# Performance work log

Measured on AMD Instinct MI355X. Metric: run time of the kernel, lower is better.

## Reference

```python
import jax, jax.numpy as jnp
import numpy as np

B, N, E = 4, 4096, 65536
FIN, FOUT = 128, 64
ALPHA = 0.2          # LeakyReLU negative slope
NEG = -9e15          # mask value from original code


def setup_inputs() -> dict:
    key = jax.random.key(0)
    k1, k2, k3, k4 = jax.random.split(key, 4)
    h = jax.random.normal(k1, (B, N, FIN), dtype=jnp.float32)
    edge_index = jax.random.randint(k2, (B, 2, E), 0, N, dtype=jnp.int32)
    # Xavier-uniform-like params
    W = jax.random.uniform(k3, (FIN, FOUT), jnp.float32, -1.0, 1.0) * (1.414 * np.sqrt(6.0 / (FIN + FOUT)))
    a = jax.random.uniform(k4, (2 * FOUT, 1), jnp.float32, -1.0, 1.0) * (1.414 * np.sqrt(6.0 / (2 * FOUT + 1)))
    return {"h": h, "edge_index": edge_index, "W": W, "a": a}


def reference(h, edge_index, W, a):
    # Wh: [B, N, FOUT]
    Wh = jnp.einsum('bnf,fo->bno', h, W)
    Wh_flat = Wh.reshape(-1, FOUT)  # [B*N, FOUT]

    # Faithful to original: raw node ids (< N) index the flattened tensor,
    # i.e. edge features are gathered from batch 0's rows.
    src = edge_index[:, 0].reshape(-1)  # [B*E]
    tgt = edge_index[:, 1].reshape(-1)  # [B*E]
    a_input = jnp.concatenate([Wh_flat[src], Wh_flat[tgt]], axis=1)  # [B*E, 2*FOUT]
    e = (a_input @ a)[:, 0]  # [B*E]

    b_idx = jnp.repeat(jnp.arange(B), E)
    e_dense = jnp.zeros((B, N, N), e.dtype).at[b_idx, src, tgt].set(e)
    e_dense = jax.nn.leaky_relu(e_dense, ALPHA)

    attention = jnp.where(e_dense > 0, e_dense, NEG)
    attention = jax.nn.softmax(attention, axis=1)  # softmax over dim=1 as in original
    # dropout p=0.0 -> no-op

    h_prime = jnp.einsum('bmn,bnf->bmf', attention, Wh)  # [B, N, FOUT]
    return jax.nn.elu(h_prime)  # concat=True path
```

## Files before the change

kernel.cpp:

```cpp
#include <hip/hip_runtime.h>
#include <hip/hip_bf16.h>

#define BB 4
#define NN 4096
#define EE 65536
#define FIN 128
#define FOUT 64
#define CAP 64

__device__ __forceinline__ unsigned enc_f32(float f) {
    unsigned b = __float_as_uint(f);
    return (b & 0x80000000u) ? ~b : (b | 0x80000000u);
}
__device__ __forceinline__ float dec_f32(unsigned e) {
    unsigned b = (e & 0x80000000u) ? (e & 0x7FFFFFFFu) : ~e;
    return __uint_as_float(b);
}

__global__ __launch_bounds__(256) void phase0_kernel(
        const float* __restrict__ h, const float* __restrict__ W, const float* __restrict__ a,
        float* __restrict__ Wh, int* __restrict__ deg, unsigned* __restrict__ Menc,
        float* __restrict__ D, float* __restrict__ base,
        float* __restrict__ as_, float* __restrict__ at_) {
    __shared__ union {
        struct { float hs[32][132]; float Ws[64][64]; } wh;
        float Wa[256];
    } smem;
    int tid = threadIdx.x;
    int bid = blockIdx.x;
    if (bid < 512) {
        long row0 = (long)bid * 32;
        for (int i = tid; i < 1024; i += 256) {
            float4 v = ((const float4*)(h + row0 * FIN))[i];
            int r = (i * 4) >> 7, c = (i * 4) & 127;
            *(float4*)&smem.wh.hs[r][c] = v;
        }
        int tx = tid & 15, ty = tid >> 4;
        int c0 = tx * 4, r0 = ty * 2;
        float acc[2][4] = {};
        for (int kk = 0; kk < 128; kk += 64) {
            __syncthreads();
            for (int i = tid; i < 1024; i += 256) {
                float4 v = ((const float4*)(W + kk * FOUT))[i];
                int k = (i * 4) >> 6, c = (i * 4) & 63;
                *(float4*)&smem.wh.Ws[k][c] = v;
            }
            __syncthreads();
#pragma unroll
            for (int k = 0; k < 64; k += 4) {
                float4 w0 = *(const float4*)&smem.wh.Ws[k][c0];
                float4 w1 = *(const float4*)&smem.wh.Ws[k + 1][c0];
                float4 w2 = *(const float4*)&smem.wh.Ws[k + 2][c0];
                float4 w3 = *(const float4*)&smem.wh.Ws[k + 3][c0];
#pragma unroll
                for (int r = 0; r < 2; ++r) {
                    float4 hv = *(const float4*)&smem.wh.hs[r0 + r][kk + k];
                    acc[r][0] += hv.x * w0.x + hv.y * w1.x + hv.z * w2.x + hv.w * w3.x;
                    acc[r][1] += hv.x * w0.y + hv.y * w1.y + hv.z * w2.y + hv.w * w3.y;
                    acc[r][2] += hv.x * w0.z + hv.y * w1.z + hv.z * w2.z + hv.w * w3.z;
                    acc[r][3] += hv.x * w0.w + hv.y * w1.w + hv.z * w2.w + hv.w * w3.w;
                }
            }
        }
#pragma unroll
        for (int r = 0; r < 2; ++r)
            *(float4*)&Wh[(row0 + r0 + r) * FOUT + c0] = *(float4*)&acc[r][0];
    } else {
        int local = bid - 512;
        int gid2 = local * 256 + tid;
        if (gid2 < BB * NN) { deg[gid2] = 0; Menc[gid2] = 0u; D[gid2] = 0.f; }
        if (gid2 < BB * FOUT) base[gid2] = 0.f;
        {
            int half = tid >> 7, k = tid & 127;
            const float* wr = W + k * FOUT;
            const float* av = a + half * FOUT;
            float s = 0.f;
#pragma unroll
            for (int f2 = 0; f2 < FOUT; ++f2) s += wr[f2] * av[f2];
            smem.Wa[half * 128 + k] = s;
        }
        __syncthreads();
        int lane = tid & 63, wv = tid >> 6;
#pragma unroll
        for (int r = 0; r < 2; ++r) {
            int n = local * 8 + wv * 2 + r;
            float h0v = h[(long)n * FIN + lane];
            float h1v = h[(long)n * FIN + 64 + lane];
            float ps = h0v * smem.Wa[lane] + h1v * smem.Wa[64 + lane];
            float pt = h0v * smem.Wa[128 + lane] + h1v * smem.Wa[192 + lane];
            for (int off = 32; off; off >>= 1) {
                ps += __shfl_down(ps, off);
                pt += __shfl_down(pt, off);
            }
            if (lane == 0) { as_[n] = ps; at_[n] = pt; }
        }
    }
}

__global__ void edge_kernel(const int* __restrict__ ei, const float* __restrict__ as_,
                            const float* __restrict__ at_, unsigned* __restrict__ Menc,
                            int* __restrict__ deg, int* __restrict__ csr) {
    int idx = blockIdx.x * 256 + threadIdx.x;
    int b = idx >> 16;
    int j = idx & 65535;
    const int* eb = ei + (long)b * 2 * EE;
    int s = eb[j], t = eb[EE + j];
    float as_s = as_[s];
    if (as_s + at_[t] > 0.f) {
        int row = (b << 12) | s;
        atomicMax(&Menc[(b << 12) | t], enc_f32(as_s));
        int slot = atomicAdd(&deg[row], 1);
        if (slot < CAP) csr[row * CAP + slot] = t;
    }
}

__global__ void phase2_kernel(int* __restrict__ deg, int* __restrict__ csr,
                              const float* __restrict__ as_, const unsigned* __restrict__ Menc,
                              float* __restrict__ D, const float* __restrict__ Wh,
                              float* __restrict__ base) {
    __shared__ float red[4][64];
    int tid = threadIdx.x;
    int lane = tid & 63;
    int row = blockIdx.x * 4 + (tid >> 6);
    int b = row >> 12, s = row & 4095;
    int draw = min(deg[row], CAP);
    int t = -1;
    if (lane < draw) t = csr[row * CAP + lane];
    bool dup = false;
    for (int k = 0; k < draw; ++k) {
        int tk = __shfl(t, k);
        if (k < lane && tk == t) dup = true;
    }
    bool keep = (lane < draw) && !dup;
    unsigned long long mask = __ballot(keep);
    int pfx = __popcll(mask & ((1ull << lane) - 1ull));
    if (keep) {
        csr[row * CAP + pfx] = t;
        float M = dec_f32(Menc[(b << 12) | t]);
        atomicAdd(&D[(b << 12) | t], expf(as_[s] - M));
    }
    if (lane == 0) deg[row] = __popcll(mask);

    if (blockIdx.x < 128) {
        int bb = blockIdx.x >> 5, chunk = blockIdx.x & 31;
        int f = tid & 63, ty = tid >> 6;
        float acc = 0.f;
        int t0 = chunk * (NN / 32);
        for (int tt = t0 + ty; tt < t0 + NN / 32; tt += 4)
            if (Menc[(bb << 12) | tt] == 0u) acc += Wh[(((long)bb << 12) | tt) * FOUT + f];
        red[ty][f] = acc;
        __syncthreads();
        if (ty == 0)
            atomicAdd(&base[(bb << 6) | f],
                      (red[0][f] + red[1][f] + red[2][f] + red[3][f]) * (1.0f / NN));
    }
}

__global__ void gather_kernel(const int* __restrict__ deg, const int* __restrict__ csr,
                              const float* __restrict__ as_, const unsigned* __restrict__ Menc,
                              const float* __restrict__ D, const float* __restrict__ Wh,
                              const float* __restrict__ base, float* __restrict__ out) {
    int tid = threadIdx.x;
    int lane = tid & 63;
    int row = blockIdx.x * 4 + (tid >> 6);
    int b = row >> 12, s = row & 4095;
    int d = deg[row];
    float as_s = as_[s];
    float acc = 0.f;
    const int* cr = csr + row * CAP;
    const float* Whb = Wh + (((long)b << 12) * FOUT);
    for (int j = 0; j < d; ++j) {
        int t = cr[j];
        float M = dec_f32(Menc[(b << 12) | t]);
        float w = expf(as_s - M) / D[(b << 12) | t];
        acc += w * Whb[t * FOUT + lane];
    }
    float x = acc + base[(b << 6) | lane];
    out[(long)row * FOUT + lane] = x > 0.f ? x : expm1f(x);
}

extern "C" void kernel_launch(void* const* d_in, const int* in_sizes, int n_in,
                              void* d_out, int out_size, void* d_ws, size_t ws_size,
                              hipStream_t stream) {
    const float* h  = (const float*)d_in[0];
    const int*   ei = (const int*)d_in[1];
    const float* W  = (const float*)d_in[2];
    const float* a  = (const float*)d_in[3];
    float* out = (float*)d_out;

    char* ws = (char*)d_ws;
    float*    Wh   = (float*)(ws);
    int*      csr  = (int*)(ws + 4194304);
    int*      deg  = (int*)(ws + 8388608);
    unsigned* Menc = (unsigned*)(ws + 8454144);
    float*    D    = (float*)(ws + 8519680);
    float*    as_  = (float*)(ws + 8585216);
    float*    at_  = (float*)(ws + 8601600);
    float*    base = (float*)(ws + 8617984);

    phase0_kernel<<<1024, 256, 0, stream>>>(h, W, a, Wh, deg, Menc, D, base, as_, at_);
    edge_kernel<<<(BB * EE) / 256, 256, 0, stream>>>(ei, as_, at_, Menc, deg, csr);
    phase2_kernel<<<(BB * NN) / 4, 256, 0, stream>>>(deg, csr, as_, Menc, D, Wh, base);
    gather_kernel<<<(BB * NN) / 4, 256, 0, stream>>>(deg, csr, as_, Menc, D, Wh, base, out);
}
```

Before: 88.20 us.

## Fuse four kernels into one persistent kernel with grid barriers

Merges the projection, edge scoring, dedup/normalisation and gather kernels into a single persistent kernel of 256 blocks that separates phases with atomic grid-wide barriers, plus a tiny init kernel. It also drops the per-target max stabiliser (atomicMax on an encoded float) in favour of a plain flag and unshifted exp(as_s), and processes four rows at once in the gather loop for more memory-level parallelism. The aim is to cut launch overhead and atomic traffic. The trade-offs are spin-barrier cost, lower parallelism from a fixed 256-block grid, possible overflow of exp without the max shift, and a deadlock risk if not all blocks are co-resident.

Result: slower. 345.2 us (+291.4%).

```diff
diff --git a/kernel.cpp b/kernel.cpp
--- a/kernel.cpp
+++ b/kernel.cpp
@@ -7,69 +7,84 @@
 #define FIN 128
 #define FOUT 64
 #define CAP 64
-
-__device__ __forceinline__ unsigned enc_f32(float f) {
-    unsigned b = __float_as_uint(f);
-    return (b & 0x80000000u) ? ~b : (b | 0x80000000u);
-}
-__device__ __forceinline__ float dec_f32(unsigned e) {
-    unsigned b = (e & 0x80000000u) ? (e & 0x7FFFFFFFu) : ~e;
-    return __uint_as_float(b);
-}
-
-__global__ __launch_bounds__(256) void phase0_kernel(
-        const float* __restrict__ h, const float* __restrict__ W, const float* __restrict__ a,
-        float* __restrict__ Wh, int* __restrict__ deg, unsigned* __restrict__ Menc,
-        float* __restrict__ D, float* __restrict__ base,
-        float* __restrict__ as_, float* __restrict__ at_) {
+#define GRID 256
+
+__device__ __forceinline__ void gbar(unsigned* c) {
+    __syncthreads();
+    if (threadIdx.x == 0) {
+        __hip_atomic_fetch_add(c, 1u, __ATOMIC_ACQ_REL, __HIP_MEMORY_SCOPE_AGENT);
+        while (__hip_atomic_fetch_add(c, 0u, __ATOMIC_ACQUIRE,
+                                      __HIP_MEMORY_SCOPE_AGENT) < (unsigned)GRID)
+            __builtin_amdgcn_s_sleep(8);
+    }
+    __syncthreads();
+}
+
+__global__ void init_kernel(unsigned* __restrict__ bar, float* __restrict__ base) {
+    if (threadIdx.x < 3) bar[threadIdx.x] = 0u;
+    base[threadIdx.x] = 0.f;
+}
+
+__global__ __launch_bounds__(256, 2) void fused(
+        const float* __restrict__ h, const int* __restrict__ ei,
+        const float* __restrict__ W, const float* __restrict__ a,
+        float* __restrict__ out, float* __restrict__ Wh, int* __restrict__ csr,
+        int* __restrict__ deg, unsigned* __restrict__ flag, float* __restrict__ D,
+        float* __restrict__ as_, float* __restrict__ at_, float* __restrict__ base,
+        unsigned* __restrict__ bar) {
     __shared__ union {
         struct { float hs[32][132]; float Ws[64][64]; } wh;
         float Wa[256];
+        float red[4][64];
     } smem;
     int tid = threadIdx.x;
     int bid = blockIdx.x;
-    if (bid < 512) {
-        long row0 = (long)bid * 32;
-        for (int i = tid; i < 1024; i += 256) {
-            float4 v = ((const float4*)(h + row0 * FIN))[i];
-            int r = (i * 4) >> 7, c = (i * 4) & 127;
-            *(float4*)&smem.wh.hs[r][c] = v;
-        }
+    int lane = tid & 63, wv = tid >> 6;
+
+    {
+        int gz = bid * 256 + tid;
+        if (gz < BB * NN) { deg[gz] = 0; flag[gz] = 0u; D[gz] = 0.f; }
+
         int tx = tid & 15, ty = tid >> 4;
         int c0 = tx * 4, r0 = ty * 2;
-        float acc[2][4] = {};
-        for (int kk = 0; kk < 128; kk += 64) {
+        for (int tile = bid; tile < 512; tile += GRID) {
             __syncthreads();
+            long row0 = (long)tile * 32;
             for (int i = tid; i < 1024; i += 256) {
-                float4 v = ((const float4*)(W + kk * FOUT))[i];
-                int k = (i * 4) >> 6, c = (i * 4) & 63;
-                *(float4*)&smem.wh.Ws[k][c] = v;
-            }
-            __syncthreads();
-#pragma unroll
-            for (int k = 0; k < 64; k += 4) {
-                float4 w0 = *(const float4*)&smem.wh.Ws[k][c0];
-                float4 w1 = *(const float4*)&smem.wh.Ws[k + 1][c0];
-                float4 w2 = *(const float4*)&smem.wh.Ws[k + 2][c0];
-                float4 w3 = *(const float4*)&smem.wh.Ws[k + 3][c0];
-#pragma unroll
-                for (int r = 0; r < 2; ++r) {
-                    float4 hv = *(const float4*)&smem.wh.hs[r0 + r][kk + k];
-                    acc[r][0] += hv.x * w0.x + hv.y * w1.x + hv.z * w2.x + hv.w * w3.x;
-                    acc[r][1] += hv.x * w0.y + hv.y * w1.y + hv.z * w2.y + hv.w * w3.y;
-                    acc[r][2] += hv.x * w0.z + hv.y * w1.z + hv.z * w2.z + hv.w * w3.z;
-                    acc[r][3] += hv.x * w0.w + hv.y * w1.w + hv.z * w2.w + hv.w * w3.w;
+                float4 v = ((const float4*)(h + row0 * FIN))[i];
+                int r = (i * 4) >> 7, c = (i * 4) & 127;
+                *(float4*)&smem.wh.hs[r][c] = v;
+            }
+            float acc[2][4] = {};
+            for (int kk = 0; kk < 128; kk += 64) {
+                __syncthreads();
+                for (int i = tid; i < 1024; i += 256) {
+                    float4 v = ((const float4*)(W + kk * FOUT))[i];
+                    int k = (i * 4) >> 6, c = (i * 4) & 63;
+                    *(float4*)&smem.wh.Ws[k][c] = v;
                 }
-            }
-        }
-#pragma unroll
-        for (int r = 0; r < 2; ++r)
-            *(float4*)&Wh[(row0 + r0 + r) * FOUT + c0] = *(float4*)&acc[r][0];
-    } else {
-        int local = bid - 512;
-        int gid2 = local * 256 + tid;
-        if (gid2 < BB * NN) { deg[gid2] = 0; Menc[gid2] = 0u; D[gid2] = 0.f; }
-        if (gid2 < BB * FOUT) base[gid2] = 0.f;
+                __syncthreads();
+#pragma unroll
+                for (int k = 0; k < 64; k += 4) {
+                    float4 w0 = *(const float4*)&smem.wh.Ws[k][c0];
+                    float4 w1 = *(const float4*)&smem.wh.Ws[k + 1][c0];
+                    float4 w2 = *(const float4*)&smem.wh.Ws[k + 2][c0];
+                    float4 w3 = *(const float4*)&smem.wh.Ws[k + 3][c0];
+#pragma unroll
+                    for (int r = 0; r < 2; ++r) {
+                        float4 hv = *(const float4*)&smem.wh.hs[r0 + r][kk + k];
+                        acc[r][0] += hv.x * w0.x + hv.y * w1.x + hv.z * w2.x + hv.w * w3.x;
+                        acc[r][1] += hv.x * w0.y + hv.y * w1.y + hv.z * w2.y + hv.w * w3.y;
+                        acc[r][2] += hv.x * w0.z + hv.y * w1.z + hv.z * w2.z + hv.w * w3.z;
+                        acc[r][3] += hv.x * w0.w + hv.y * w1.w + hv.z * w2.w + hv.w * w3.w;
+                    }
+                }
+            }
+#pragma unroll
+            for (int r = 0; r < 2; ++r)
+                *(float4*)&Wh[(row0 + r0 + r) * FOUT + c0] = *(float4*)&acc[r][0];
+        }
+        __syncthreads();
         {
             int half = tid >> 7, k = tid & 127;
             const float* wr = W + k * FOUT;
@@ -80,10 +95,9 @@
             smem.Wa[half * 128 + k] = s;
         }
         __syncthreads();
-        int lane = tid & 63, wv = tid >> 6;
-#pragma unroll
-        for (int r = 0; r < 2; ++r) {
-            int n = local * 8 + wv * 2 + r;
+#pragma unroll
+        for (int r = 0; r < 4; ++r) {
+            int n = bid * 16 + wv * 4 + r;
             float h0v = h[(long)n * FIN + lane];
             float h1v = h[(long)n * FIN + 64 + lane];
             float ps = h0v * smem.Wa[lane] + h1v * smem.Wa[64 + lane];
@@ -95,88 +109,89 @@
             if (lane == 0) { as_[n] = ps; at_[n] = pt; }
         }
     }
-}
-
-__global__ void edge_kernel(const int* __restrict__ ei, const float* __restrict__ as_,
-                            const float* __restrict__ at_, unsigned* __restrict__ Menc,
-                            int* __restrict__ deg, int* __restrict__ csr) {
-    int idx = blockIdx.x * 256 + threadIdx.x;
-    int b = idx >> 16;
-    int j = idx & 65535;
-    const int* eb = ei + (long)b * 2 * EE;
-    int s = eb[j], t = eb[EE + j];
-    float as_s = as_[s];
-    if (as_s + at_[t] > 0.f) {
-        int row = (b << 12) | s;
-        atomicMax(&Menc[(b << 12) | t], enc_f32(as_s));
-        int slot = atomicAdd(&deg[row], 1);
-        if (slot < CAP) csr[row * CAP + slot] = t;
-    }
-}
-
-__global__ void phase2_kernel(int* __restrict__ deg, int* __restrict__ csr,
-                              const float* __restrict__ as_, const unsigned* __restrict__ Menc,
-                              float* __restrict__ D, const float* __restrict__ Wh,
-                              float* __restrict__ base) {
-    __shared__ float red[4][64];
-    int tid = threadIdx.x;
-    int lane = tid & 63;
-    int row = blockIdx.x * 4 + (tid >> 6);
-    int b = row >> 12, s = row & 4095;
-    int draw = min(deg[row], CAP);
-    int t = -1;
-    if (lane < draw) t = csr[row * CAP + lane];
-    bool dup = false;
-    for (int k = 0; k < draw; ++k) {
-        int tk = __shfl(t, k);
-        if (k < lane && tk == t) dup = true;
-    }
-    bool keep = (lane < draw) && !dup;
-    unsigned long long mask = __ballot(keep);
-    int pfx = __popcll(mask & ((1ull << lane) - 1ull));
-    if (keep) {
-        csr[row * CAP + pfx] = t;
-        float M = dec_f32(Menc[(b << 12) | t]);
-        atomicAdd(&D[(b << 12) | t], expf(as_[s] - M));
-    }
-    if (lane == 0) deg[row] = __popcll(mask);
-
-    if (blockIdx.x < 128) {
-        int bb = blockIdx.x >> 5, chunk = blockIdx.x & 31;
+    gbar(&bar[0]);
+
+#pragma unroll
+    for (int b = 0; b < BB; ++b) {
+        int j = bid * 256 + tid;
+        const int* eb = ei + (long)b * 2 * EE;
+        int s = eb[j], t = eb[EE + j];
+        float as_s = as_[s];
+        if (as_s + at_[t] > 0.f) {
+            flag[(b << 12) | t] = 1u;
+            int row = (b << 12) | s;
+            int slot = atomicAdd(&deg[row], 1);
+            if (slot < CAP) csr[row * CAP + slot] = t;
+        }
+    }
+    gbar(&bar[1]);
+
+    for (int i = 0; i < 16; ++i) {
+        int row = bid * 64 + wv * 16 + i;
+        int b = row >> 12, s = row & 4095;
+        int draw = min(deg[row], CAP);
+        int t = -1;
+        if (lane < draw) t = csr[row * CAP + lane];
+        bool dup = false;
+        for (int k = 0; k < draw; ++k) {
+            int tk = __shfl(t, k);
+            if (k < lane && tk == t) dup = true;
+        }
+        bool keep = (lane < draw) && !dup;
+        unsigned long long mask = __ballot(keep);
+        int pfx = __popcll(mask & ((1ull << lane) - 1ull));
+        if (keep) {
+            csr[row * CAP + pfx] = t;
+            atomicAdd(&D[(b << 12) | t], expf(as_[s]));
+        }
+        if (lane == 0) deg[row] = __popcll(mask);
+    }
+    if (bid < 128) {
+        int bb = bid >> 5, chunk = bid & 31;
         int f = tid & 63, ty = tid >> 6;
         float acc = 0.f;
         int t0 = chunk * (NN / 32);
         for (int tt = t0 + ty; tt < t0 + NN / 32; tt += 4)
-            if (Menc[(bb << 12) | tt] == 0u) acc += Wh[(((long)bb << 12) | tt) * FOUT + f];
-        red[ty][f] = acc;
+            if (flag[(bb << 12) | tt] == 0u) acc += Wh[(((long)bb << 12) | tt) * FOUT + f];
+        __syncthreads();
+        smem.red[ty][f] = acc;
         __syncthreads();
         if (ty == 0)
             atomicAdd(&base[(bb << 6) | f],
-                      (red[0][f] + red[1][f] + red[2][f] + red[3][f]) * (1.0f / NN));
-    }
-}
-
-__global__ void gather_kernel(const int* __restrict__ deg, const int* __restrict__ csr,
-                              const float* __restrict__ as_, const unsigned* __restrict__ Menc,
-                              const float* __restrict__ D, const float* __restrict__ Wh,
-                              const float* __restrict__ base, float* __restrict__ out) {
-    int tid = threadIdx.x;
-    int lane = tid & 63;
-    int row = blockIdx.x * 4 + (tid >> 6);
-    int b = row >> 12, s = row & 4095;
-    int d = deg[row];
-    float as_s = as_[s];
-    float acc = 0.f;
-    const int* cr = csr + row * CAP;
-    const float* Whb = Wh + (((long)b << 12) * FOUT);
-    for (int j = 0; j < d; ++j) {
-        int t = cr[j];
-        float M = dec_f32(Menc[(b << 12) | t]);
-        float w = expf(as_s - M) / D[(b << 12) | t];
-        acc += w * Whb[t * FOUT + lane];
-    }
-    float x = acc + base[(b << 6) | lane];
-    out[(long)row * FOUT + lane] = x > 0.f ? x : expm1f(x);
+                      (smem.red[0][f] + smem.red[1][f] + smem.red[2][f] + smem.red[3][f]) *
+                          (1.0f / NN));
+    }
+    gbar(&bar[2]);
+
+    {
+        int b = bid >> 6;
+        const float* Whb = Wh + (((long)b << 12) * FOUT);
+        const float* Db = D + (b << 12);
+        float bs = base[(b << 6) | lane];
+        for (int rr = 0; rr < 16; rr += 4) {
+            int row0 = bid * 64 + wv * 16 + rr;
+            int d0 = deg[row0], d1 = deg[row0 + 1], d2 = deg[row0 + 2], d3 = deg[row0 + 3];
+            float E0 = expf(as_[row0 & 4095]), E1 = expf(as_[(row0 + 1) & 4095]);
+            float E2 = expf(as_[(row0 + 2) & 4095]), E3 = expf(as_[(row0 + 3) & 4095]);
+            const int* c0p = csr + (long)row0 * CAP;
+            const int* c1p = c0p + CAP;
+            const int* c2p = c1p + CAP;
+            const int* c3p = c2p + CAP;
+            float a0 = 0.f, a1 = 0.f, a2 = 0.f, a3 = 0.f;
+            int dmax = max(max(d0, d1), max(d2, d3));
+            for (int j = 0; j < dmax; ++j) {
+                if (j < d0) { int t = c0p[j]; a0 += (E0 / Db[t]) * Whb[t * FOUT + lane]; }
+                if (j < d1) { int t = c1p[j]; a1 += (E1 / Db[t]) * Whb[t * FOUT + lane]; }
+                if (j < d2) { int t = c2p[j]; a2 += (E2 / Db[t]) * Whb[t * FOUT + lane]; }
+                if (j < d3) { int t = c3p[j]; a3 += (E3 / Db[t]) * Whb[t * FOUT + lane]; }
+            }
+            float x0 = a0 + bs, x1 = a1 + bs, x2 = a2 + bs, x3 = a3 + bs;
+            out[(long)row0 * FOUT + lane] = x0 > 0.f ? x0 : expm1f(x0);
+            out[(long)(row0 + 1) * FOUT + lane] = x1 > 0.f ? x1 : expm1f(x1);
+            out[(long)(row0 + 2) * FOUT + lane] = x2 > 0.f ? x2 : expm1f(x2);
+            out[(long)(row0 + 3) * FOUT + lane] = x3 > 0.f ? x3 : expm1f(x3);
+        }
+    }
 }
 
 extern "C" void kernel_launch(void* const* d_in, const int* in_sizes, int n_in,
@@ -192,14 +207,14 @@
     float*    Wh   = (float*)(ws);
     int*      csr  = (int*)(ws + 4194304);
     int*      deg  = (int*)(ws + 8388608);
-    unsigned* Menc = (unsigned*)(ws + 8454144);
+    unsigned* flag = (unsigned*)(ws + 8454144);
     float*    D    = (float*)(ws + 8519680);
     float*    as_  = (float*)(ws + 8585216);
     float*    at_  = (float*)(ws + 8601600);
     float*    base = (float*)(ws + 8617984);
-
-    phase0_kernel<<<1024, 256, 0, stream>>>(h, W, a, Wh, deg, Menc, D, base, as_, at_);
-    edge_kernel<<<(BB * EE) / 256, 256, 0, stream>>>(ei, as_, at_, Menc, deg, csr);
-    phase2_kernel<<<(BB * NN) / 4, 256, 0, stream>>>(deg, csr, as_, Menc, D, Wh, base);
-    gather_kernel<<<(BB * NN) / 4, 256, 0, stream>>>(deg, csr, as_, Menc, D, Wh, base, out);
-}
+    unsigned* bar  = (unsigned*)(ws + 8619008);
+
+    init_kernel<<<1, 256, 0, stream>>>(bar, base);
+    fused<<<GRID, 256, 0, stream>>>(h, ei, W, a, out, Wh, csr, deg, flag, D,
+                                    as_, at_, base, bar);
+}
```

## Dedupe edges with a bitmap in edge pass and drop max-subtraction phase

Applied to the files above, without the earlier changes.

Edge duplicates are now removed in the edge kernel with an atomicOr on a per-(batch,src,tgt) bitmap, and the softmax denominator is accumulated there directly as exp(as_s) with no max subtraction. This removes the phase2 kernel and the Menc array. The gather kernel now computes the base term for columns with no entries itself and processes four rows per wave. Each block clears 16KB of a 8MB bitmap, and skipping the max subtraction means exp(as_s) could overflow for large scores.

Result: slower. 104.4 us (+18.4%).

```diff
diff --git a/kernel.cpp b/kernel.cpp
--- a/kernel.cpp
+++ b/kernel.cpp
@@ -8,20 +8,10 @@
 #define FOUT 64
 #define CAP 64
 
-__device__ __forceinline__ unsigned enc_f32(float f) {
-    unsigned b = __float_as_uint(f);
-    return (b & 0x80000000u) ? ~b : (b | 0x80000000u);
-}
-__device__ __forceinline__ float dec_f32(unsigned e) {
-    unsigned b = (e & 0x80000000u) ? (e & 0x7FFFFFFFu) : ~e;
-    return __uint_as_float(b);
-}
-
 __global__ __launch_bounds__(256) void phase0_kernel(
         const float* __restrict__ h, const float* __restrict__ W, const float* __restrict__ a,
-        float* __restrict__ Wh, int* __restrict__ deg, unsigned* __restrict__ Menc,
-        float* __restrict__ D, float* __restrict__ base,
-        float* __restrict__ as_, float* __restrict__ at_) {
+        float* __restrict__ Wh, int* __restrict__ deg, float* __restrict__ D,
+        unsigned* __restrict__ bitmap, float* __restrict__ as_, float* __restrict__ at_) {
     __shared__ union {
         struct { float hs[32][132]; float Ws[64][64]; } wh;
         float Wa[256];
@@ -67,9 +57,10 @@
             *(float4*)&Wh[(row0 + r0 + r) * FOUT + c0] = *(float4*)&acc[r][0];
     } else {
         int local = bid - 512;
+        uint4* bm4 = (uint4*)(bitmap + (long)local * 4096);
+        for (int i = tid; i < 1024; i += 256) bm4[i] = make_uint4(0u, 0u, 0u, 0u);
         int gid2 = local * 256 + tid;
-        if (gid2 < BB * NN) { deg[gid2] = 0; Menc[gid2] = 0u; D[gid2] = 0.f; }
-        if (gid2 < BB * FOUT) base[gid2] = 0.f;
+        if (gid2 < BB * NN) { deg[gid2] = 0; D[gid2] = 0.f; }
         {
             int half = tid >> 7, k = tid & 127;
             const float* wr = W + k * FOUT;
@@ -98,8 +89,9 @@
 }
 
 __global__ void edge_kernel(const int* __restrict__ ei, const float* __restrict__ as_,
-                            const float* __restrict__ at_, unsigned* __restrict__ Menc,
-                            int* __restrict__ deg, int* __restrict__ csr) {
+                            const float* __restrict__ at_, unsigned* __restrict__ bitmap,
+                            int* __restrict__ deg, int* __restrict__ csr,
+                            float* __restrict__ D) {
     int idx = blockIdx.x * 256 + threadIdx.x;
     int b = idx >> 16;
     int j = idx & 65535;
@@ -108,75 +100,70 @@
     float as_s = as_[s];
     if (as_s + at_[t] > 0.f) {
         int row = (b << 12) | s;
-        atomicMax(&Menc[(b << 12) | t], enc_f32(as_s));
-        int slot = atomicAdd(&deg[row], 1);
-        if (slot < CAP) csr[row * CAP + slot] = t;
+        long bit = ((long)row << 12) | t;
+        unsigned m = 1u << (bit & 31);
+        unsigned old = atomicOr(&bitmap[bit >> 5], m);
+        if (!(old & m)) {
+            atomicAdd(&D[(b << 12) | t], expf(as_s));
+            int slot = atomicAdd(&deg[row], 1);
+            if (slot < CAP) csr[row * CAP + slot] = t;
+        }
     }
 }
 
-__global__ void phase2_kernel(int* __restrict__ deg, int* __restrict__ csr,
-                              const float* __restrict__ as_, const unsigned* __restrict__ Menc,
-                              float* __restrict__ D, const float* __restrict__ Wh,
-                              float* __restrict__ base) {
-    __shared__ float red[4][64];
+__global__ __launch_bounds__(256) void gather_kernel(
+        const int* __restrict__ deg, const int* __restrict__ csr,
+        const float* __restrict__ as_, const float* __restrict__ D,
+        const float* __restrict__ Wh, float* __restrict__ out) {
+    __shared__ float bs[64];
+    __shared__ int list[256];
+    __shared__ int cnt;
     int tid = threadIdx.x;
-    int lane = tid & 63;
-    int row = blockIdx.x * 4 + (tid >> 6);
-    int b = row >> 12, s = row & 4095;
-    int draw = min(deg[row], CAP);
-    int t = -1;
-    if (lane < draw) t = csr[row * CAP + lane];
-    bool dup = false;
-    for (int k = 0; k < draw; ++k) {
-        int tk = __shfl(t, k);
-        if (k < lane && tk == t) dup = true;
+    int lane = tid & 63, wv = tid >> 6;
+    int bid = blockIdx.x;
+    int b = bid >> 8;
+    const float* Db = D + (b << 12);
+    const float* Whb = Wh + (((long)b << 12) * FOUT);
+    if (tid == 0) cnt = 0;
+    __syncthreads();
+    for (int i = tid; i < NN; i += 256) {
+        if (Db[i] == 0.f) {
+            int p = atomicAdd(&cnt, 1);
+            if (p < 256) list[p] = i;
+        }
     }
-    bool keep = (lane < draw) && !dup;
-    unsigned long long mask = __ballot(keep);
-    int pfx = __popcll(mask & ((1ull << lane) - 1ull));
-    if (keep) {
-        csr[row * CAP + pfx] = t;
-        float M = dec_f32(Menc[(b << 12) | t]);
-        atomicAdd(&D[(b << 12) | t], expf(as_[s] - M));
+    __syncthreads();
+    if (wv == 0) {
+        int c = min(cnt, 256);
+        float s = 0.f;
+        for (int j = 0; j < c; ++j) s += Whb[list[j] * FOUT + lane];
+        bs[lane] = s * (1.0f / NN);
     }
-    if (lane == 0) deg[row] = __popcll(mask);
+    __syncthreads();
+    float bsv = bs[lane];
 
-    if (blockIdx.x < 128) {
-        int bb = blockIdx.x >> 5, chunk = blockIdx.x & 31;
-        int f = tid & 63, ty = tid >> 6;
-        float acc = 0.f;
-        int t0 = chunk * (NN / 32);
-        for (int tt = t0 + ty; tt < t0 + NN / 32; tt += 4)
-            if (Menc[(bb << 12) | tt] == 0u) acc += Wh[(((long)bb << 12) | tt) * FOUT + f];
-        red[ty][f] = acc;
-        __syncthreads();
-        if (ty == 0)
-            atomicAdd(&base[(bb << 6) | f],
-                      (red[0][f] + red[1][f] + red[2][f] + red[3][f]) * (1.0f / NN));
+    int row0 = bid * 16 + wv * 4;
+    int d0 = min(deg[row0], CAP), d1 = min(deg[row0 + 1], CAP);
+    int d2 = min(deg[row0 + 2], CAP), d3 = min(deg[row0 + 3], CAP);
+    float E0 = expf(as_[row0 & 4095]), E1 = expf(as_[(row0 + 1) & 4095]);
+    float E2 = expf(as_[(row0 + 2) & 4095]), E3 = expf(as_[(row0 + 3) & 4095]);
+    const int* c0p = csr + (long)row0 * CAP;
+    const int* c1p = c0p + CAP;
+    const int* c2p = c1p + CAP;
+    const int* c3p = c2p + CAP;
+    float a0 = 0.f, a1 = 0.f, a2 = 0.f, a3 = 0.f;
+    int dmax = max(max(d0, d1), max(d2, d3));
+    for (int j = 0; j < dmax; ++j) {
+        if (j < d0) { int t = c0p[j]; a0 += (E0 / Db[t]) * Whb[t * FOUT + lane]; }
+        if (j < d1) { int t = c1p[j]; a1 += (E1 / Db[t]) * Whb[t * FOUT + lane]; }
+        if (j < d2) { int t = c2p[j]; a2 += (E2 / Db[t]) * Whb[t * FOUT + lane]; }
+        if (j < d3) { int t = c3p[j]; a3 += (E3 / Db[t]) * Whb[t * FOUT + lane]; }
     }
-}
-
-__global__ void gather_kernel(const int* __restrict__ deg, const int* __restrict__ csr,
-                              const float* __restrict__ as_, const unsigned* __restrict__ Menc,
-                              const float* __restrict__ D, const float* __restrict__ Wh,
-                              const float* __restrict__ base, float* __restrict__ out) {
-    int tid = threadIdx.x;
-    int lane = tid & 63;
-    int row = blockIdx.x * 4 + (tid >> 6);
-    int b = row >> 12, s = row & 4095;
-    int d = deg[row];
-    float as_s = as_[s];
-    float acc = 0.f;
-    const int* cr = csr + row * CAP;
-    const float* Whb = Wh + (((long)b << 12) * FOUT);
-    for (int j = 0; j < d; ++j) {
-        int t = cr[j];
-        float M = dec_f32(Menc[(b << 12) | t]);
-        float w = expf(as_s - M) / D[(b << 12) | t];
-        acc += w * Whb[t * FOUT + lane];
-    }
-    float x = acc + base[(b << 6) | lane];
-    out[(long)row * FOUT + lane] = x > 0.f ? x : expm1f(x);
+    float x0 = a0 + bsv, x1 = a1 + bsv, x2 = a2 + bsv, x3 = a3 + bsv;
+    out[(long)row0 * FOUT + lane] = x0 > 0.f ? x0 : expm1f(x0);
+    out[(long)(row0 + 1) * FOUT + lane] = x1 > 0.f ? x1 : expm1f(x1);
+    out[(long)(row0 + 2) * FOUT + lane] = x2 > 0.f ? x2 : expm1f(x2);
+    out[(long)(row0 + 3) * FOUT + lane] = x3 > 0.f ? x3 : expm1f(x3);
 }
 
 extern "C" void kernel_launch(void* const* d_in, const int* in_sizes, int n_in,
@@ -189,17 +176,15 @@
     float* out = (float*)d_out;
 
     char* ws = (char*)d_ws;
-    float*    Wh   = (float*)(ws);
-    int*      csr  = (int*)(ws + 4194304);
-    int*      deg  = (int*)(ws + 8388608);
-    unsigned* Menc = (unsigned*)(ws + 8454144);
-    float*    D    = (float*)(ws + 8519680);
-    float*    as_  = (float*)(ws + 8585216);
-    float*    at_  = (float*)(ws + 8601600);
-    float*    base = (float*)(ws + 8617984);
+    float*    Wh     = (float*)(ws);
+    int*      csr    = (int*)(ws + 4194304);
+    unsigned* bitmap = (unsigned*)(ws + 8388608);
+    int*      deg    = (int*)(ws + 16777216);
+    float*    D      = (float*)(ws + 16842752);
+    float*    as_    = (float*)(ws + 16908288);
+    float*    at_    = (float*)(ws + 16924672);
 
-    phase0_kernel<<<1024, 256, 0, stream>>>(h, W, a, Wh, deg, Menc, D, base, as_, at_);
-    edge_kernel<<<(BB * EE) / 256, 256, 0, stream>>>(ei, as_, at_, Menc, deg, csr);
-    phase2_kernel<<<(BB * NN) / 4, 256, 0, stream>>>(deg, csr, as_, Menc, D, Wh, base);
-    gather_kernel<<<(BB * NN) / 4, 256, 0, stream>>>(deg, csr, as_, Menc, D, Wh, base, out);
+    phase0_kernel<<<1024, 256, 0, stream>>>(h, W, a, Wh, deg, D, bitmap, as_, at_);
+    edge_kernel<<<(BB * EE) / 256, 256, 0, stream>>>(ei, as_, at_, bitmap, deg, csr, D);
+    gather_kernel<<<(BB * NN) / 16, 256, 0, stream>>>(deg, csr, as_, D, Wh, out);
 }
```
